# Kernel optimization log

Measured on AMD Instinct MI355X. Metric: run time of the kernel, lower is better.

Reference implementation:

```python
import jax, jax.numpy as jnp
import numpy as np

B, S, H, D = 2, 2048, 16, 128

def setup_inputs() -> dict:
    key = jax.random.key(0)
    kq, kk, kv = jax.random.split(key, 3)
    query = jax.random.normal(kq, (B, S, H, D), dtype=jnp.float32)
    key_t = jax.random.normal(kk, (B, S, H, D), dtype=jnp.float32)
    value = jax.random.normal(kv, (B, S, H, D), dtype=jnp.float32)
    return {"query": query, "key": key_t, "value": value}

def reference(query, key, value):
    # Single-device equivalent: SeqAllToAll4D is identity (world_size=1),
    # ring flash attention == exact softmax attention.
    # Layout [B, S, H, D] (flash-attn convention), non-causal, no dropout.
    scale = 1.0 / jnp.sqrt(jnp.asarray(query.shape[-1], query.dtype))
    # scores: [B, H, Sq, Sk]
    scores = jnp.einsum("bqhd,bkhd->bhqk", query, key) * scale
    probs = jax.nn.softmax(scores, axis=-1)
    out = jnp.einsum("bhqk,bkhd->bqhd", probs, value)
    return out
```

## Files before the change

### kernel.cpp

```cpp
#include <hip/hip_runtime.h>
#include <hip/hip_bf16.h>

#define NB 2
#define NS 2048
#define NH 16
#define ND 128
#define SROW (NH*ND)

#define QBLK 128
#define KBLK 64
#define NTHR 512

#define KSTR 136
#define VSTR 72

typedef __attribute__((ext_vector_type(4))) float f32x4;
typedef __attribute__((ext_vector_type(8))) __bf16 bf16x8;
typedef __attribute__((ext_vector_type(8))) short s16x8;
typedef __attribute__((ext_vector_type(4))) short s16x4;

__device__ __forceinline__ short f2bf(float f) {
  union { float f; unsigned u; } v; v.f = f;
  unsigned r = v.u + 0x7fffu + ((v.u >> 16) & 1u);
  return (short)(r >> 16);
}

__global__ __launch_bounds__(256)
void prep_k(const float* __restrict__ K, short* __restrict__ Kb) {
  const float sc = 0.08838834764831845f * 1.4426950408889634f;
  size_t i = (size_t)blockIdx.x * 256 + threadIdx.x;
  int g = (int)(i & 31);
  size_t row = i >> 5;
  int h = (int)(row & (NH - 1));
  size_t bs = row >> 4;
  int s = (int)(bs & (NS - 1));
  int b = (int)(bs >> 11);
  float4 x = *(const float4*)(K + row * ND + g * 4);
  s16x4 w = { f2bf(x.x * sc), f2bf(x.y * sc), f2bf(x.z * sc), f2bf(x.w * sc) };
  *(s16x4*)(Kb + ((size_t)(b * NH + h) * NS + s) * ND + g * 4) = w;
}

__global__ __launch_bounds__(256)
void prep_v(const float* __restrict__ V, short* __restrict__ VT) {
  __shared__ short tile[64 * 72];
  int gid = blockIdx.x;
  int st = gid & 31;
  int dt = (gid >> 5) & 1;
  int bh = gid >> 6;
  int b = bh >> 4, h = bh & 15;
  int s0 = st * 64, d0 = dt * 64;
  const float* src = V + ((size_t)b * NS * NH + h) * ND;
#pragma unroll
  for (int it = 0; it < 4; ++it) {
    int idx = threadIdx.x + it * 256;
    int r = idx >> 4;
    int c = (idx & 15) * 4;
    float4 x = *(const float4*)(src + (size_t)(s0 + r) * SROW + d0 + c);
    s16x4 w = { f2bf(x.x), f2bf(x.y), f2bf(x.z), f2bf(x.w) };
    *(s16x4*)&tile[r * 72 + c] = w;
  }
  __syncthreads();
  short* dst = VT + (size_t)bh * ND * NS;
#pragma unroll
  for (int it = 0; it < 2; ++it) {
    int idx = threadIdx.x + it * 256;
    int dr = idx >> 3;
    int c8 = (idx & 7) * 8;
    s16x8 w;
#pragma unroll
    for (int j = 0; j < 8; ++j) w[j] = tile[(c8 + j) * 72 + dr];
    *(s16x8*)(dst + (size_t)(d0 + dr) * NS + s0 + c8) = w;
  }
}

__global__ __launch_bounds__(NTHR, 4)
void attn_fwd4(const float* __restrict__ Q, const short* __restrict__ Kb,
               const short* __restrict__ VTb, float* __restrict__ O)
{
  __shared__ __align__(16) short kbuf[2][KBLK * KSTR];
  __shared__ __align__(16) short vbuf[2][ND * VSTR];

  const int tid  = threadIdx.x;
  const int wave = tid >> 6;
  const int lane = tid & 63;
  const int g    = lane >> 4;
  const int lr   = lane & 15;

  const int nqb = NS / QBLK;
  const int qb  = blockIdx.x % nqb;
  const int bh  = blockIdx.x / nqb;
  const int b   = bh / NH;
  const int h   = bh % NH;

  const float* Qb = Q + ((size_t)b * NS * NH + h) * ND;
  float*       Ob = O + ((size_t)b * NS * NH + h) * ND;
  const short* Kbh = Kb  + (size_t)bh * NS * ND;
  const short* Vbh = VTb + (size_t)bh * ND * NS;

  const int q0 = qb * QBLK + wave * 16;

  bf16x8 qf[4];
  {
    const float* qp = Qb + (size_t)(q0 + lr) * SROW;
#pragma unroll
    for (int kc = 0; kc < 4; ++kc) {
      const int d0 = kc * 32 + g * 8;
      float4 a = *(const float4*)(qp + d0);
      float4 c = *(const float4*)(qp + d0 + 4);
      s16x8 f;
      f[0] = f2bf(a.x); f[1] = f2bf(a.y); f[2] = f2bf(a.z); f[3] = f2bf(a.w);
      f[4] = f2bf(c.x); f[5] = f2bf(c.y); f[6] = f2bf(c.z); f[7] = f2bf(c.w);
      qf[kc] = __builtin_bit_cast(bf16x8, f);
    }
  }

  f32x4 oacc[8];
#pragma unroll
  for (int dc = 0; dc < 8; ++dc) oacc[dc] = (f32x4){0.f, 0.f, 0.f, 0.f};
  float mrun  = -1e30f;
  float lpart = 0.f;

  s16x8 kreg[2], vreg[2];

  int vc = tid & 7;
  int ksb = vc >> 2, q4 = vc & 3;
  const int vcol0 = ksb * 32 + ((q4 * 2) & 3) * 8 + (q4 >> 1) * 4;

#define LOAD_TILES(KV0)                                                        \
  {                                                                            \
    _Pragma("unroll")                                                          \
    for (int it = 0; it < 2; ++it) {                                           \
      int idx = tid + it * NTHR;                                               \
      int kr = idx >> 4, kc = (idx & 15) * 8;                                  \
      kreg[it] = *(const s16x8*)(Kbh + (size_t)((KV0) + kr) * ND + kc);        \
      int vr = idx >> 3, vq = (idx & 7) * 8;                                   \
      vreg[it] = *(const s16x8*)(Vbh + (size_t)vr * NS + (KV0) + vq);          \
    }                                                                          \
  }

  LOAD_TILES(0);

  for (int kt = 0; kt < NS / KBLK; ++kt) {
    short* kl = kbuf[kt & 1];
    short* vl = vbuf[kt & 1];

#pragma unroll
    for (int it = 0; it < 2; ++it) {
      int idx = tid + it * NTHR;
      int kr = idx >> 4, kc = (idx & 15) * 8;
      *(s16x8*)&kl[kr * KSTR + kc] = kreg[it];
      int vr = idx >> 3;
      s16x8 v = vreg[it];
      s16x4 vlo = __builtin_shufflevector(v, v, 0, 1, 2, 3);
      s16x4 vhi = __builtin_shufflevector(v, v, 4, 5, 6, 7);
      *(s16x4*)&vl[vr * VSTR + vcol0]     = vlo;
      *(s16x4*)&vl[vr * VSTR + vcol0 + 8] = vhi;
    }
    __syncthreads();

    if (kt + 1 < NS / KBLK) LOAD_TILES((kt + 1) * KBLK);

    f32x4 sacc[4];
    __builtin_amdgcn_s_setprio(1);
#pragma unroll
    for (int nb = 0; nb < 4; ++nb) {
      f32x4 acc = {0.f, 0.f, 0.f, 0.f};
#pragma unroll
      for (int kc = 0; kc < 4; ++kc) {
        bf16x8 kf = *(const bf16x8*)&kl[(nb * 16 + lr) * KSTR + kc * 32 + g * 8];
        acc = __builtin_amdgcn_mfma_f32_16x16x32_bf16(kf, qf[kc], acc, 0, 0, 0);
      }
      sacc[nb] = acc;
    }
    __builtin_amdgcn_s_setprio(0);

    float mloc = sacc[0][0];
#pragma unroll
    for (int nb = 0; nb < 4; ++nb)
#pragma unroll
      for (int i = 0; i < 4; ++i) mloc = fmaxf(mloc, sacc[nb][i]);

    if (__any(mloc > mrun + 10.0f)) {
      float m2 = mloc;
      m2 = fmaxf(m2, __shfl_xor(m2, 16));
      m2 = fmaxf(m2, __shfl_xor(m2, 32));
      float mnew = fmaxf(mrun, m2);
      float alpha = exp2f(mrun - mnew);
      mrun = mnew;
      lpart *= alpha;
      float ar[4];
#pragma unroll
      for (int i = 0; i < 4; ++i) ar[i] = __shfl(alpha, g * 4 + i);
#pragma unroll
      for (int dc = 0; dc < 8; ++dc)
#pragma unroll
        for (int i = 0; i < 4; ++i) oacc[dc][i] *= ar[i];
    }

#pragma unroll
    for (int nb = 0; nb < 4; ++nb)
#pragma unroll
      for (int i = 0; i < 4; ++i) {
        float p = exp2f(sacc[nb][i] - mrun);
        sacc[nb][i] = p;
        lpart += p;
      }

    s16x8 p0, p1;
#pragma unroll
    for (int i = 0; i < 4; ++i) {
      p0[i]     = f2bf(sacc[0][i]);
      p0[i + 4] = f2bf(sacc[1][i]);
      p1[i]     = f2bf(sacc[2][i]);
      p1[i + 4] = f2bf(sacc[3][i]);
    }
    bf16x8 pf0 = __builtin_bit_cast(bf16x8, p0);
    bf16x8 pf1 = __builtin_bit_cast(bf16x8, p1);

    __builtin_amdgcn_s_setprio(1);
#pragma unroll
    for (int dc = 0; dc < 8; ++dc) {
      bf16x8 vf0 = *(const bf16x8*)&vl[(dc * 16 + lr) * VSTR + g * 8];
      oacc[dc] = __builtin_amdgcn_mfma_f32_16x16x32_bf16(pf0, vf0, oacc[dc], 0, 0, 0);
      bf16x8 vf1 = *(const bf16x8*)&vl[(dc * 16 + lr) * VSTR + 32 + g * 8];
      oacc[dc] = __builtin_amdgcn_mfma_f32_16x16x32_bf16(pf1, vf1, oacc[dc], 0, 0, 0);
    }
    __builtin_amdgcn_s_setprio(0);
  }

  float l = lpart;
  l += __shfl_xor(l, 16);
  l += __shfl_xor(l, 32);
  float inv = 1.0f / l;
  float* op = Ob + (size_t)q0 * SROW;
#pragma unroll
  for (int i = 0; i < 4; ++i) {
    int m = g * 4 + i;
    float invm = __shfl(inv, m);
#pragma unroll
    for (int dc = 0; dc < 8; ++dc)
      op[(size_t)m * SROW + dc * 16 + lr] = oacc[dc][i] * invm;
  }
#undef LOAD_TILES
}

__global__ __launch_bounds__(256, 2)
void attn_fwd_legacy(const float* __restrict__ Q, const float* __restrict__ K,
                     const float* __restrict__ V, float* __restrict__ O)
{
  __shared__ __align__(16) short k_lds[KBLK * KSTR];
  __shared__ __align__(16) short vt_lds[ND * VSTR];
  __shared__ __align__(16) short p_lds[4 * 16 * 72];

  const int tid = threadIdx.x;
  const int wave = tid >> 6;
  const int lane = tid & 63;
  const int g = lane >> 4;
  const int lr = lane & 15;

  const int nqb = NS / 64;
  const int qb = blockIdx.x % nqb;
  const int bh = blockIdx.x / nqb;
  const int b = bh / NH;
  const int h = bh % NH;

  const float scale = 0.08838834764831845f * 1.4426950408889634f;
  const size_t base = ((size_t)b * NS * NH + h) * ND;
  const float* Qb = Q + base;
  const float* Kbp = K + base;
  const float* Vb = V + base;
  float* Ob = O + base;
  const int q0 = qb * 64 + wave * 16;

  bf16x8 qf[4];
  {
    const float* qp = Qb + (size_t)(q0 + lr) * SROW;
#pragma unroll
    for (int kc = 0; kc < 4; ++kc) {
      const int d0 = kc * 32 + g * 8;
      float4 a = *(const float4*)(qp + d0);
      float4 c = *(const float4*)(qp + d0 + 4);
      s16x8 f;
      f[0] = f2bf(a.x * scale); f[1] = f2bf(a.y * scale);
      f[2] = f2bf(a.z * scale); f[3] = f2bf(a.w * scale);
      f[4] = f2bf(c.x * scale); f[5] = f2bf(c.y * scale);
      f[6] = f2bf(c.z * scale); f[7] = f2bf(c.w * scale);
      qf[kc] = __builtin_bit_cast(bf16x8, f);
    }
  }

  f32x4 oacc[8];
#pragma unroll
  for (int dc = 0; dc < 8; ++dc) oacc[dc] = (f32x4){0.f, 0.f, 0.f, 0.f};
  float mrun[4] = {-1e30f, -1e30f, -1e30f, -1e30f};
  float lrun[4] = {0.f, 0.f, 0.f, 0.f};

  for (int kt = 0; kt < NS / KBLK; ++kt) {
    const int kv0 = kt * KBLK;
    __syncthreads();
#pragma unroll
    for (int it = 0; it < 8; ++it) {
      int idx = tid + it * 256;
      int r = idx >> 5;
      int c = (idx & 31) << 2;
      float4 x = *(const float4*)(Kbp + (size_t)(kv0 + r) * SROW + c);
      s16x4 w = { f2bf(x.x), f2bf(x.y), f2bf(x.z), f2bf(x.w) };
      *(s16x4*)&k_lds[r * KSTR + c] = w;
    }
#pragma unroll
    for (int it = 0; it < 2; ++it) {
      int sub = tid + it * 256;
      int skv = (sub >> 5) << 2;
      int sd = (sub & 31) << 2;
      const float* vp = Vb + (size_t)(kv0 + skv) * SROW + sd;
      float4 r0 = *(const float4*)(vp);
      float4 r1 = *(const float4*)(vp + SROW);
      float4 r2 = *(const float4*)(vp + 2 * SROW);
      float4 r3 = *(const float4*)(vp + 3 * SROW);
      s16x4 w0 = { f2bf(r0.x), f2bf(r1.x), f2bf(r2.x), f2bf(r3.x) };
      s16x4 w1 = { f2bf(r0.y), f2bf(r1.y), f2bf(r2.y), f2bf(r3.y) };
      s16x4 w2 = { f2bf(r0.z), f2bf(r1.z), f2bf(r2.z), f2bf(r3.z) };
      s16x4 w3 = { f2bf(r0.w), f2bf(r1.w), f2bf(r2.w), f2bf(r3.w) };
      *(s16x4*)&vt_lds[(sd + 0) * VSTR + skv] = w0;
      *(s16x4*)&vt_lds[(sd + 1) * VSTR + skv] = w1;
      *(s16x4*)&vt_lds[(sd + 2) * VSTR + skv] = w2;
      *(s16x4*)&vt_lds[(sd + 3) * VSTR + skv] = w3;
    }
    __syncthreads();

    f32x4 sacc[4];
#pragma unroll
    for (int nb = 0; nb < 4; ++nb) {
      f32x4 acc = {0.f, 0.f, 0.f, 0.f};
#pragma unroll
      for (int kc = 0; kc < 4; ++kc) {
        bf16x8 kf = *(const bf16x8*)&k_lds[(nb * 16 + lr) * KSTR + kc * 32 + g * 8];
        acc = __builtin_amdgcn_mfma_f32_16x16x32_bf16(qf[kc], kf, acc, 0, 0, 0);
      }
      sacc[nb] = acc;
    }

    float alpha[4];
#pragma unroll
    for (int i = 0; i < 4; ++i) {
      float m = fmaxf(fmaxf(sacc[0][i], sacc[1][i]), fmaxf(sacc[2][i], sacc[3][i]));
#pragma unroll
      for (int off = 1; off < 16; off <<= 1) m = fmaxf(m, __shfl_xor(m, off));
      float mnew = fmaxf(mrun[i], m);
      alpha[i] = exp2f(mrun[i] - mnew);
      mrun[i] = mnew;
    }
    float rsum[4] = {0.f, 0.f, 0.f, 0.f};
#pragma unroll
    for (int nb = 0; nb < 4; ++nb)
#pragma unroll
      for (int i = 0; i < 4; ++i) {
        float p = exp2f(sacc[nb][i] - mrun[i]);
        sacc[nb][i] = p;
        rsum[i] += p;
      }
#pragma unroll
    for (int i = 0; i < 4; ++i) {
#pragma unroll
      for (int off = 1; off < 16; off <<= 1) rsum[i] += __shfl_xor(rsum[i], off);
      lrun[i] = lrun[i] * alpha[i] + rsum[i];
    }
#pragma unroll
    for (int dc = 0; dc < 8; ++dc)
#pragma unroll
      for (int i = 0; i < 4; ++i) oacc[dc][i] *= alpha[i];

    short* pw = &p_lds[wave * 16 * 72];
#pragma unroll
    for (int nb = 0; nb < 4; ++nb)
#pragma unroll
      for (int i = 0; i < 4; ++i)
        pw[(g * 4 + i) * 72 + nb * 16 + lr] = f2bf(sacc[nb][i]);

    bf16x8 pf0 = *(const bf16x8*)&pw[lr * 72 + g * 8];
    bf16x8 pf1 = *(const bf16x8*)&pw[lr * 72 + 32 + g * 8];

#pragma unroll
    for (int dc = 0; dc < 8; ++dc) {
      bf16x8 vf0 = *(const bf16x8*)&vt_lds[(dc * 16 + lr) * VSTR + g * 8];
      oacc[dc] = __builtin_amdgcn_mfma_f32_16x16x32_bf16(pf0, vf0, oacc[dc], 0, 0, 0);
      bf16x8 vf1 = *(const bf16x8*)&vt_lds[(dc * 16 + lr) * VSTR + 32 + g * 8];
      oacc[dc] = __builtin_amdgcn_mfma_f32_16x16x32_bf16(pf1, vf1, oacc[dc], 0, 0, 0);
    }
  }

  float* op = Ob + (size_t)q0 * SROW;
#pragma unroll
  for (int i = 0; i < 4; ++i) {
    float inv = 1.0f / lrun[i];
    int m = g * 4 + i;
#pragma unroll
    for (int dc = 0; dc < 8; ++dc)
      op[(size_t)m * SROW + dc * 16 + lr] = oacc[dc][i] * inv;
  }
}

extern "C" void kernel_launch(void* const* d_in, const int* in_sizes, int n_in,
                              void* d_out, int out_size, void* d_ws, size_t ws_size,
                              hipStream_t stream) {
  const float* Q = (const float*)d_in[0];
  const float* K = (const float*)d_in[1];
  const float* V = (const float*)d_in[2];
  float* O = (float*)d_out;

  const size_t elems = (size_t)NB * NS * NH * ND;
  const size_t need = 2 * elems * sizeof(short);

  if (ws_size >= need) {
    short* Kb = (short*)d_ws;
    short* VT = Kb + elems;
    hipLaunchKernelGGL(prep_k, dim3((unsigned)(elems / 4 / 256)), dim3(256), 0, stream, K, Kb);
    hipLaunchKernelGGL(prep_v, dim3(NB * NH * (NS / 64) * (ND / 64)), dim3(256), 0, stream, V, VT);
    hipLaunchKernelGGL(attn_fwd4, dim3(NB * NH * (NS / QBLK)), dim3(NTHR), 0, stream, Q, Kb, VT, O);
  } else {
    hipLaunchKernelGGL(attn_fwd_legacy, dim3(NB * NH * (NS / 64)), dim3(256), 0, stream, Q, K, V, O);
  }
}
```

Before: 119.0 us.

## Give each wave two 16-row query tiles to reuse K/V LDS fragments

```diff
diff --git a/kernel.cpp b/kernel.cpp
--- a/kernel.cpp
+++ b/kernel.cpp
@@ -9,13 +9,15 @@
 
 #define QBLK 128
 #define KBLK 64
-#define NTHR 512
+#define NTHR 256
+#define NT   (NS/KBLK)
 
 #define KSTR 136
 #define VSTR 72
 
 typedef __attribute__((ext_vector_type(4))) float f32x4;
 typedef __attribute__((ext_vector_type(8))) __bf16 bf16x8;
+typedef __attribute__((ext_vector_type(4))) __bf16 bf16x4;
 typedef __attribute__((ext_vector_type(8))) short s16x8;
 typedef __attribute__((ext_vector_type(4))) short s16x4;
 
@@ -36,8 +38,8 @@
   int s = (int)(bs & (NS - 1));
   int b = (int)(bs >> 11);
   float4 x = *(const float4*)(K + row * ND + g * 4);
-  s16x4 w = { f2bf(x.x * sc), f2bf(x.y * sc), f2bf(x.z * sc), f2bf(x.w * sc) };
-  *(s16x4*)(Kb + ((size_t)(b * NH + h) * NS + s) * ND + g * 4) = w;
+  bf16x4 w = { (__bf16)(x.x * sc), (__bf16)(x.y * sc), (__bf16)(x.z * sc), (__bf16)(x.w * sc) };
+  *(bf16x4*)(Kb + ((size_t)(b * NH + h) * NS + s) * ND + g * 4) = w;
 }
 
 __global__ __launch_bounds__(256)
@@ -56,8 +58,8 @@
     int r = idx >> 4;
     int c = (idx & 15) * 4;
     float4 x = *(const float4*)(src + (size_t)(s0 + r) * SROW + d0 + c);
-    s16x4 w = { f2bf(x.x), f2bf(x.y), f2bf(x.z), f2bf(x.w) };
-    *(s16x4*)&tile[r * 72 + c] = w;
+    bf16x4 w = { (__bf16)x.x, (__bf16)x.y, (__bf16)x.z, (__bf16)x.w };
+    *(bf16x4*)&tile[r * 72 + c] = w;
   }
   __syncthreads();
   short* dst = VT + (size_t)bh * ND * NS;
@@ -73,8 +75,8 @@
   }
 }
 
-__global__ __launch_bounds__(NTHR, 4)
-void attn_fwd4(const float* __restrict__ Q, const short* __restrict__ Kb,
+__global__ __launch_bounds__(NTHR, 2)
+void attn_fwd5(const float* __restrict__ Q, const short* __restrict__ Kb,
                const short* __restrict__ VTb, float* __restrict__ O)
 {
   __shared__ __align__(16) short kbuf[2][KBLK * KSTR];
@@ -97,151 +99,176 @@
   const short* Kbh = Kb  + (size_t)bh * NS * ND;
   const short* Vbh = VTb + (size_t)bh * ND * NS;
 
-  const int q0 = qb * QBLK + wave * 16;
-
-  bf16x8 qf[4];
-  {
-    const float* qp = Qb + (size_t)(q0 + lr) * SROW;
+  const int wq0 = qb * QBLK + wave * 32;
+
+  bf16x8 qf[2][4];
+#pragma unroll
+  for (int qt = 0; qt < 2; ++qt) {
+    const float* qp = Qb + (size_t)(wq0 + qt * 16 + lr) * SROW;
 #pragma unroll
     for (int kc = 0; kc < 4; ++kc) {
       const int d0 = kc * 32 + g * 8;
       float4 a = *(const float4*)(qp + d0);
       float4 c = *(const float4*)(qp + d0 + 4);
-      s16x8 f;
-      f[0] = f2bf(a.x); f[1] = f2bf(a.y); f[2] = f2bf(a.z); f[3] = f2bf(a.w);
-      f[4] = f2bf(c.x); f[5] = f2bf(c.y); f[6] = f2bf(c.z); f[7] = f2bf(c.w);
-      qf[kc] = __builtin_bit_cast(bf16x8, f);
-    }
-  }
-
-  f32x4 oacc[8];
-#pragma unroll
-  for (int dc = 0; dc < 8; ++dc) oacc[dc] = (f32x4){0.f, 0.f, 0.f, 0.f};
-  float mrun  = -1e30f;
-  float lpart = 0.f;
-
-  s16x8 kreg[2], vreg[2];
-
-  int vc = tid & 7;
-  int ksb = vc >> 2, q4 = vc & 3;
+      bf16x8 f;
+      f[0] = (__bf16)a.x; f[1] = (__bf16)a.y; f[2] = (__bf16)a.z; f[3] = (__bf16)a.w;
+      f[4] = (__bf16)c.x; f[5] = (__bf16)c.y; f[6] = (__bf16)c.z; f[7] = (__bf16)c.w;
+      qf[qt][kc] = f;
+    }
+  }
+
+  f32x4 oacc[2][8];
+#pragma unroll
+  for (int qt = 0; qt < 2; ++qt)
+#pragma unroll
+    for (int dc = 0; dc < 8; ++dc) oacc[qt][dc] = (f32x4){0.f, 0.f, 0.f, 0.f};
+  float mrun[2]  = {-1e30f, -1e30f};
+  float lpart[2] = {0.f, 0.f};
+
+  const int vc = tid & 7;
+  const int ksb = vc >> 2, q4 = vc & 3;
   const int vcol0 = ksb * 32 + ((q4 * 2) & 3) * 8 + (q4 >> 1) * 4;
-
-#define LOAD_TILES(KV0)                                                        \
-  {                                                                            \
-    _Pragma("unroll")                                                          \
-    for (int it = 0; it < 2; ++it) {                                           \
-      int idx = tid + it * NTHR;                                               \
-      int kr = idx >> 4, kc = (idx & 15) * 8;                                  \
-      kreg[it] = *(const s16x8*)(Kbh + (size_t)((KV0) + kr) * ND + kc);        \
-      int vr = idx >> 3, vq = (idx & 7) * 8;                                   \
-      vreg[it] = *(const s16x8*)(Vbh + (size_t)vr * NS + (KV0) + vq);          \
-    }                                                                          \
-  }
-
-  LOAD_TILES(0);
-
-  for (int kt = 0; kt < NS / KBLK; ++kt) {
+  const int klo = (tid >> 4) * KSTR + (tid & 15) * 8;
+  const int vlo = (tid >> 3) * VSTR + vcol0;
+
+  const short* kp = Kbh + (tid >> 4) * ND + (tid & 15) * 8;
+  const short* vp = Vbh + (size_t)(tid >> 3) * NS + vc * 8;
+
+  s16x8 kreg[4], vreg[4];
+#pragma unroll
+  for (int it = 0; it < 4; ++it) {
+    kreg[it] = *(const s16x8*)(kp + it * (16 * ND));
+    vreg[it] = *(const s16x8*)(vp + (size_t)it * (32 * NS));
+  }
+  kp += KBLK * ND;
+  vp += KBLK;
+
+  for (int kt = 0; kt < NT; ++kt) {
     short* kl = kbuf[kt & 1];
     short* vl = vbuf[kt & 1];
 
 #pragma unroll
-    for (int it = 0; it < 2; ++it) {
-      int idx = tid + it * NTHR;
-      int kr = idx >> 4, kc = (idx & 15) * 8;
-      *(s16x8*)&kl[kr * KSTR + kc] = kreg[it];
-      int vr = idx >> 3;
+    for (int it = 0; it < 4; ++it) {
+      *(s16x8*)&kl[klo + it * (16 * KSTR)] = kreg[it];
       s16x8 v = vreg[it];
-      s16x4 vlo = __builtin_shufflevector(v, v, 0, 1, 2, 3);
-      s16x4 vhi = __builtin_shufflevector(v, v, 4, 5, 6, 7);
-      *(s16x4*)&vl[vr * VSTR + vcol0]     = vlo;
-      *(s16x4*)&vl[vr * VSTR + vcol0 + 8] = vhi;
+      s16x4 vlo4 = __builtin_shufflevector(v, v, 0, 1, 2, 3);
+      s16x4 vhi4 = __builtin_shufflevector(v, v, 4, 5, 6, 7);
+      *(s16x4*)&vl[vlo + it * (32 * VSTR)]     = vlo4;
+      *(s16x4*)&vl[vlo + it * (32 * VSTR) + 8] = vhi4;
     }
     __syncthreads();
 
-    if (kt + 1 < NS / KBLK) LOAD_TILES((kt + 1) * KBLK);
-
-    f32x4 sacc[4];
+    if (kt + 1 < NT) {
+#pragma unroll
+      for (int it = 0; it < 4; ++it) {
+        kreg[it] = *(const s16x8*)(kp + it * (16 * ND));
+        vreg[it] = *(const s16x8*)(vp + (size_t)it * (32 * NS));
+      }
+      kp += KBLK * ND;
+      vp += KBLK;
+    }
+
+    f32x4 sacc[2][4];
     __builtin_amdgcn_s_setprio(1);
 #pragma unroll
     for (int nb = 0; nb < 4; ++nb) {
-      f32x4 acc = {0.f, 0.f, 0.f, 0.f};
+      f32x4 a0 = {0.f, 0.f, 0.f, 0.f};
+      f32x4 a1 = {0.f, 0.f, 0.f, 0.f};
 #pragma unroll
       for (int kc = 0; kc < 4; ++kc) {
         bf16x8 kf = *(const bf16x8*)&kl[(nb * 16 + lr) * KSTR + kc * 32 + g * 8];
-        acc = __builtin_amdgcn_mfma_f32_16x16x32_bf16(kf, qf[kc], acc, 0, 0, 0);
-      }
-      sacc[nb] = acc;
+        a0 = __builtin_amdgcn_mfma_f32_16x16x32_bf16(kf, qf[0][kc], a0, 0, 0, 0);
+        a1 = __builtin_amdgcn_mfma_f32_16x16x32_bf16(kf, qf[1][kc], a1, 0, 0, 0);
+      }
+      sacc[0][nb] = a0;
+      sacc[1][nb] = a1;
     }
     __builtin_amdgcn_s_setprio(0);
 
-    float mloc = sacc[0][0];
-#pragma unroll
-    for (int nb = 0; nb < 4; ++nb)
-#pragma unroll
-      for (int i = 0; i < 4; ++i) mloc = fmaxf(mloc, sacc[nb][i]);
-
-    if (__any(mloc > mrun + 10.0f)) {
-      float m2 = mloc;
-      m2 = fmaxf(m2, __shfl_xor(m2, 16));
-      m2 = fmaxf(m2, __shfl_xor(m2, 32));
-      float mnew = fmaxf(mrun, m2);
-      float alpha = exp2f(mrun - mnew);
-      mrun = mnew;
-      lpart *= alpha;
-      float ar[4];
-#pragma unroll
-      for (int i = 0; i < 4; ++i) ar[i] = __shfl(alpha, g * 4 + i);
-#pragma unroll
-      for (int dc = 0; dc < 8; ++dc)
-#pragma unroll
-        for (int i = 0; i < 4; ++i) oacc[dc][i] *= ar[i];
-    }
-
-#pragma unroll
-    for (int nb = 0; nb < 4; ++nb)
+    float mloc[2];
+#pragma unroll
+    for (int qt = 0; qt < 2; ++qt) {
+      float m = sacc[qt][0][0];
+#pragma unroll
+      for (int nb = 0; nb < 4; ++nb)
+#pragma unroll
+        for (int i = 0; i < 4; ++i) m = fmaxf(m, sacc[qt][nb][i]);
+      mloc[qt] = m;
+    }
+    bool need = (mloc[0] > mrun[0] + 10.0f) || (mloc[1] > mrun[1] + 10.0f);
+    if (__any(need)) {
+#pragma unroll
+      for (int qt = 0; qt < 2; ++qt) {
+        float m2 = mloc[qt];
+        m2 = fmaxf(m2, __shfl_xor(m2, 16));
+        m2 = fmaxf(m2, __shfl_xor(m2, 32));
+        float mnew = fmaxf(mrun[qt], m2);
+        float alpha = exp2f(mrun[qt] - mnew);
+        mrun[qt] = mnew;
+        lpart[qt] *= alpha;
+        float ar[4];
+#pragma unroll
+        for (int i = 0; i < 4; ++i) ar[i] = __shfl(alpha, g * 4 + i);
+#pragma unroll
+        for (int dc = 0; dc < 8; ++dc)
+#pragma unroll
+          for (int i = 0; i < 4; ++i) oacc[qt][dc][i] *= ar[i];
+      }
+    }
+#pragma unroll
+    for (int qt = 0; qt < 2; ++qt)
+#pragma unroll
+      for (int nb = 0; nb < 4; ++nb)
+#pragma unroll
+        for (int i = 0; i < 4; ++i) {
+          float p = exp2f(sacc[qt][nb][i] - mrun[qt]);
+          sacc[qt][nb][i] = p;
+          lpart[qt] += p;
+        }
+
+    bf16x8 pf[2][2];
+#pragma unroll
+    for (int qt = 0; qt < 2; ++qt) {
+      bf16x8 t0, t1;
 #pragma unroll
       for (int i = 0; i < 4; ++i) {
-        float p = exp2f(sacc[nb][i] - mrun);
-        sacc[nb][i] = p;
-        lpart += p;
-      }
-
-    s16x8 p0, p1;
-#pragma unroll
-    for (int i = 0; i < 4; ++i) {
-      p0[i]     = f2bf(sacc[0][i]);
-      p0[i + 4] = f2bf(sacc[1][i]);
-      p1[i]     = f2bf(sacc[2][i]);
-      p1[i + 4] = f2bf(sacc[3][i]);
-    }
-    bf16x8 pf0 = __builtin_bit_cast(bf16x8, p0);
-    bf16x8 pf1 = __builtin_bit_cast(bf16x8, p1);
+        t0[i]     = (__bf16)sacc[qt][0][i];
+        t0[i + 4] = (__bf16)sacc[qt][1][i];
+        t1[i]     = (__bf16)sacc[qt][2][i];
+        t1[i + 4] = (__bf16)sacc[qt][3][i];
+      }
+      pf[qt][0] = t0;
+      pf[qt][1] = t1;
+    }
 
     __builtin_amdgcn_s_setprio(1);
 #pragma unroll
     for (int dc = 0; dc < 8; ++dc) {
       bf16x8 vf0 = *(const bf16x8*)&vl[(dc * 16 + lr) * VSTR + g * 8];
-      oacc[dc] = __builtin_amdgcn_mfma_f32_16x16x32_bf16(pf0, vf0, oacc[dc], 0, 0, 0);
       bf16x8 vf1 = *(const bf16x8*)&vl[(dc * 16 + lr) * VSTR + 32 + g * 8];
-      oacc[dc] = __builtin_amdgcn_mfma_f32_16x16x32_bf16(pf1, vf1, oacc[dc], 0, 0, 0);
+      oacc[0][dc] = __builtin_amdgcn_mfma_f32_16x16x32_bf16(pf[0][0], vf0, oacc[0][dc], 0, 0, 0);
+      oacc[1][dc] = __builtin_amdgcn_mfma_f32_16x16x32_bf16(pf[1][0], vf0, oacc[1][dc], 0, 0, 0);
+      oacc[0][dc] = __builtin_amdgcn_mfma_f32_16x16x32_bf16(pf[0][1], vf1, oacc[0][dc], 0, 0, 0);
+      oacc[1][dc] = __builtin_amdgcn_mfma_f32_16x16x32_bf16(pf[1][1], vf1, oacc[1][dc], 0, 0, 0);
     }
     __builtin_amdgcn_s_setprio(0);
   }
 
-  float l = lpart;
-  l += __shfl_xor(l, 16);
-  l += __shfl_xor(l, 32);
-  float inv = 1.0f / l;
-  float* op = Ob + (size_t)q0 * SROW;
-#pragma unroll
-  for (int i = 0; i < 4; ++i) {
-    int m = g * 4 + i;
-    float invm = __shfl(inv, m);
-#pragma unroll
-    for (int dc = 0; dc < 8; ++dc)
-      op[(size_t)m * SROW + dc * 16 + lr] = oacc[dc][i] * invm;
-  }
-#undef LOAD_TILES
+#pragma unroll
+  for (int qt = 0; qt < 2; ++qt) {
+    float l = lpart[qt];
+    l += __shfl_xor(l, 16);
+    l += __shfl_xor(l, 32);
+    float inv = 1.0f / l;
+#pragma unroll
+    for (int i = 0; i < 4; ++i) {
+      float invm = __shfl(inv, g * 4 + i);
+      float* orow = Ob + (size_t)(wq0 + qt * 16 + g * 4 + i) * SROW;
+#pragma unroll
+      for (int dc = 0; dc < 8; ++dc)
+        orow[dc * 16 + lr] = oacc[qt][dc][i] * invm;
+    }
+  }
 }
 
 __global__ __launch_bounds__(256, 2)
@@ -416,7 +443,7 @@
     short* VT = Kb + elems;
     hipLaunchKernelGGL(prep_k, dim3((unsigned)(elems / 4 / 256)), dim3(256), 0, stream, K, Kb);
     hipLaunchKernelGGL(prep_v, dim3(NB * NH * (NS / 64) * (ND / 64)), dim3(256), 0, stream, V, VT);
-    hipLaunchKernelGGL(attn_fwd4, dim3(NB * NH * (NS / QBLK)), dim3(NTHR), 0, stream, Q, Kb, VT, O);
+    hipLaunchKernelGGL(attn_fwd5, dim3(NB * NH * (NS / QBLK)), dim3(NTHR), 0, stream, Q, Kb, VT, O);
   } else {
     hipLaunchKernelGGL(attn_fwd_legacy, dim3(NB * NH * (NS / 64)), dim3(256), 0, stream, Q, K, V, O);
   }
```

New measurement: 107.9 us. 9.3% less time.
